# Performance work log

Hardware: AMD Instinct MI355X
Metric: run time of the kernel (lower is better)

Reference implementation:

```python
import jax, jax.numpy as jnp
import numpy as np

N = 50000      # nodes
E = 800000     # edges
IN = 128       # in_dim
EMB = 32       # emb_dim
ED = 8         # edge_dim
L = 4          # num_layers
B = 64         # num graphs in batch
OUT = 10       # out_dim
EPS = 1e-5


def setup_inputs() -> dict:
    key = jax.random.key(0)
    ks = jax.random.split(key, 16)
    f32 = jnp.float32
    def nrm(k, shape, scale):
        return jax.random.normal(k, shape, dtype=f32) * scale
    inp = {}
    inp['x'] = nrm(ks[0], (N, IN), 1.0)
    inp['edge_index'] = jax.random.randint(ks[1], (2, E), 0, N)
    inp['edge_attr'] = nrm(ks[2], (E, ED), 1.0)
    inp['batch'] = jnp.sort(jax.random.randint(ks[3], (N,), 0, B))
    # lin_in
    inp['lin_in_w'] = nrm(ks[4], (IN, EMB), 0.05)
    inp['lin_in_b'] = jnp.zeros((EMB,), f32)
    # per-layer message MLP: Linear(2e+ed->e), BN, ReLU, Linear(e->e), BN, ReLU
    inp['msg_w1'] = nrm(ks[5], (L, 2 * EMB + ED, EMB), 0.1)
    inp['msg_b1'] = jnp.zeros((L, EMB), f32)
    inp['msg_g1'] = jnp.ones((L, EMB), f32)
    inp['msg_be1'] = jnp.zeros((L, EMB), f32)
    inp['msg_w2'] = nrm(ks[6], (L, EMB, EMB), 0.1)
    inp['msg_b2'] = jnp.zeros((L, EMB), f32)
    inp['msg_g2'] = jnp.ones((L, EMB), f32)
    inp['msg_be2'] = jnp.zeros((L, EMB), f32)
    # per-layer update MLP: Linear(2e->e), BN, ReLU, Linear(e->e), BN, ReLU
    inp['upd_w1'] = nrm(ks[7], (L, 2 * EMB, EMB), 0.1)
    inp['upd_b1'] = jnp.zeros((L, EMB), f32)
    inp['upd_g1'] = jnp.ones((L, EMB), f32)
    inp['upd_be1'] = jnp.zeros((L, EMB), f32)
    inp['upd_w2'] = nrm(ks[8], (L, EMB, EMB), 0.1)
    inp['upd_b2'] = jnp.zeros((L, EMB), f32)
    inp['upd_g2'] = jnp.ones((L, EMB), f32)
    inp['upd_be2'] = jnp.zeros((L, EMB), f32)
    # lin_pred
    inp['pred_w'] = nrm(ks[9], (EMB, OUT), 0.1)
    inp['pred_b'] = jnp.zeros((OUT,), f32)
    return inp


def _bn(x, g, b):
    # BatchNorm1d in training mode: batch stats over dim 0 (biased variance)
    mu = jnp.mean(x, axis=0)
    var = jnp.mean(jnp.square(x - mu), axis=0)
    return (x - mu) * jax.lax.rsqrt(var + EPS) * g + b


def reference(x, edge_attr, lin_in_w, lin_in_b,
              msg_w1, msg_b1, msg_g1, msg_be1, msg_w2, msg_b2, msg_g2, msg_be2,
              upd_w1, upd_b1, upd_g1, upd_be1, upd_w2, upd_b2, upd_g2, upd_be2,
              pred_w, pred_b, edge_index, batch):
    src = edge_index[0]  # h_j source nodes
    dst = edge_index[1]  # h_i target nodes (aggregation index)
    h = x @ lin_in_w + lin_in_b  # [N, EMB]
    for i in range(L):
        # message: gather + concat + MLP(BN,ReLU)x2 over edges
        msg_in = jnp.concatenate([h[dst], h[src], edge_attr], axis=-1)  # [E, 2e+ed]
        m = jax.nn.relu(_bn(msg_in @ msg_w1[i] + msg_b1[i], msg_g1[i], msg_be1[i]))
        m = jax.nn.relu(_bn(m @ msg_w2[i] + msg_b2[i], msg_g2[i], msg_be2[i]))
        # aggregate: scatter-add by destination
        aggr = jax.ops.segment_sum(m, dst, num_segments=N)  # [N, EMB]
        # update: concat + MLP(BN,ReLU)x2
        u = jnp.concatenate([h, aggr], axis=-1)  # [N, 2e]
        u = jax.nn.relu(_bn(u @ upd_w1[i] + upd_b1[i], upd_g1[i], upd_be1[i]))
        u = jax.nn.relu(_bn(u @ upd_w2[i] + upd_b2[i], upd_g2[i], upd_be2[i]))
        h = u + h  # residual in MPNNModel.get_embeddings
    # global mean pool
    sums = jax.ops.segment_sum(h, batch, num_segments=B)
    counts = jax.ops.segment_sum(jnp.ones((N,), h.dtype), batch, num_segments=B)
    h_graph = sums / jnp.maximum(counts, 1.0)[:, None]
    return h_graph @ pred_w + pred_b  # [B, OUT]
```

## Files before the change

### kernel.cpp

```cpp
#include <hip/hip_runtime.h>
#include <cstddef>

#define N_NODES 50000
#define N_EDGES 800000
#define IN_DIM  128
#define EMB     32
#define ED      8
#define NLAYERS 4
#define NB      64
#define OUTD    10
#define EPS_BN  1e-5f

#define EDGE_GRID 3125
#define NODE_GRID 196
#define NODE4_GRID 782
#define AU_GRID   6250
#define NTILE_N   3125
#define LIN_GRID  782
#define ST_TPW    4
#define ST_GRID   3125
#define MSG2_TPW  4
#define MSG2_GRID 3125

#define SREP 4

typedef short bf16x8 __attribute__((ext_vector_type(8)));
typedef float f32x4  __attribute__((ext_vector_type(4)));


__device__ __forceinline__ unsigned short f2bf(float x) {
  union { float f; unsigned u; } v; v.f = x;
  unsigned b = v.u + 0x7FFFu + ((v.u >> 16) & 1u);
  return (unsigned short)(b >> 16);
}
__device__ __forceinline__ float bf2f(unsigned short s) {
  union { unsigned u; float f; } v; v.u = ((unsigned)s) << 16;
  return v.f;
}

__device__ __forceinline__ void coef_from_stats(const float* __restrict__ stats_stage,
                                                const float* __restrict__ g,
                                                const float* __restrict__ be,
                                                float inv_count, float* __restrict__ cf) {
  if (threadIdx.x < EMB) {
    const int c = threadIdx.x;
    float s = 0.f, ss = 0.f;
#pragma unroll
    for (int r = 0; r < SREP; ++r) {
      s  += stats_stage[r*64 + c];
      ss += stats_stage[r*64 + EMB + c];
    }
    const float mu  = s * inv_count;
    const float var = ss * inv_count - mu*mu;
    const float a = g[c] * rsqrtf(var + EPS_BN);
    cf[c] = a;
    cf[EMB + c] = fmaf(-mu, a, be[c]);
  }
  __syncthreads();
}

__device__ __forceinline__ void wave_stats_atomic(float ts[8], float tss[8],
                                                  float* __restrict__ lds_s,
                                                  float* __restrict__ lds_q,
                                                  float* __restrict__ stats_stage) {
  const int lane = threadIdx.x & 63;
  const int wv   = threadIdx.x >> 6;
#pragma unroll
  for (int j = 0; j < 8; ++j) {
    float a = ts[j], b = tss[j];
#pragma unroll
    for (int o = 32; o > 0; o >>= 1) {
      a += __shfl_down(a, o, 64);
      b += __shfl_down(b, o, 64);
    }
    ts[j] = a; tss[j] = b;
  }
  if (lane == 0) {
#pragma unroll
    for (int j = 0; j < 8; ++j) {
      lds_s[wv*8 + j] = ts[j];
      lds_q[wv*8 + j] = tss[j];
    }
  }
  __syncthreads();
  if (threadIdx.x < 64) {
    const float v = (threadIdx.x < 32) ? lds_s[threadIdx.x] : lds_q[threadIdx.x - 32];
    atomicAdd(stats_stage + ((blockIdx.x & (SREP-1)) << 6) + threadIdx.x, v);
  }
}

#define HSTRIDE 40

__global__ __launch_bounds__(256) void k_lin_in_pq(
    const float* __restrict__ x, const float* __restrict__ w, const float* __restrict__ b,
    const float* __restrict__ w1, const float* __restrict__ b1, const int* __restrict__ ei,
    float* __restrict__ h, unsigned short* __restrict__ p, unsigned short* __restrict__ q,
    int* __restrict__ cnt)
{
  __shared__ __align__(16) unsigned short lds_hb[4][16*HSTRIDE];
  __shared__ __align__(16) unsigned short lds_pq[4][16*HSTRIDE];
  const int lane = threadIdx.x & 63;
  const int wv   = threadIdx.x >> 6;
  const int n0i  = lane & 15;
  const int quad = lane >> 4;

  const int tile = blockIdx.x*4 + wv;
  if (tile < NTILE_N) {
    const int r0 = tile*16;
    bf16x8 BwL[4], BwH[4];
#pragma unroll
    for (int kb = 0; kb < 4; ++kb) {
#pragma unroll
      for (int j = 0; j < 8; ++j) {
        const int k = kb*32 + quad*8 + j;
        BwL[kb][j] = (short)f2bf(w[k*EMB + n0i]);
        BwH[kb][j] = (short)f2bf(w[k*EMB + 16 + n0i]);
      }
    }
    f32x4 accL = {0.f,0.f,0.f,0.f};
    f32x4 accH = {0.f,0.f,0.f,0.f};
#pragma unroll
    for (int kb = 0; kb < 4; ++kb) {
      const float4 xa = *(const float4*)(x + (size_t)(r0 + n0i)*IN_DIM + kb*32 + quad*8);
      const float4 xb = *(const float4*)(x + (size_t)(r0 + n0i)*IN_DIM + kb*32 + quad*8 + 4);
      bf16x8 A;
      A[0] = (short)f2bf(xa.x); A[1] = (short)f2bf(xa.y);
      A[2] = (short)f2bf(xa.z); A[3] = (short)f2bf(xa.w);
      A[4] = (short)f2bf(xb.x); A[5] = (short)f2bf(xb.y);
      A[6] = (short)f2bf(xb.z); A[7] = (short)f2bf(xb.w);
      accL = __builtin_amdgcn_mfma_f32_16x16x32_bf16(A, BwL[kb], accL, 0, 0, 0);
      accH = __builtin_amdgcn_mfma_f32_16x16x32_bf16(A, BwH[kb], accH, 0, 0, 0);
    }
    const float bL = b[n0i], bH = b[16 + n0i];
#pragma unroll
    for (int r = 0; r < 4; ++r) {
      const int row = quad*4 + r;
      const float vL = accL[r] + bL;
      const float vH = accH[r] + bH;
      h[(size_t)(r0 + row)*EMB + n0i]      = vL;
      h[(size_t)(r0 + row)*EMB + 16 + n0i] = vH;
      lds_hb[wv][row*HSTRIDE + n0i]      = f2bf(vL);
      lds_hb[wv][row*HSTRIDE + 16 + n0i] = f2bf(vH);
    }
    bf16x8 A2;
#pragma unroll
    for (int j = 0; j < 8; ++j)
      A2[j] = (short)lds_hb[wv][n0i*HSTRIDE + quad*8 + j];
    bf16x8 BpL, BpH, BqL, BqH;
#pragma unroll
    for (int j = 0; j < 8; ++j) {
      const int k = quad*8 + j;
      BpL[j] = (short)f2bf(w1[k*EMB + n0i]);
      BpH[j] = (short)f2bf(w1[k*EMB + 16 + n0i]);
      BqL[j] = (short)f2bf(w1[(EMB + k)*EMB + n0i]);
      BqH[j] = (short)f2bf(w1[(EMB + k)*EMB + 16 + n0i]);
    }
    const f32x4 z4 = {0.f,0.f,0.f,0.f};
    f32x4 pL = __builtin_amdgcn_mfma_f32_16x16x32_bf16(A2, BpL, z4, 0, 0, 0);
    f32x4 pH = __builtin_amdgcn_mfma_f32_16x16x32_bf16(A2, BpH, z4, 0, 0, 0);
    f32x4 qL = __builtin_amdgcn_mfma_f32_16x16x32_bf16(A2, BqL, z4, 0, 0, 0);
    f32x4 qH = __builtin_amdgcn_mfma_f32_16x16x32_bf16(A2, BqH, z4, 0, 0, 0);
    const float b1L = b1[n0i], b1H = b1[16 + n0i];
#pragma unroll
    for (int r = 0; r < 4; ++r) {
      const int row = quad*4 + r;
      lds_pq[wv][row*HSTRIDE + n0i]      = f2bf(pL[r] + b1L);
      lds_pq[wv][row*HSTRIDE + 16 + n0i] = f2bf(pH[r] + b1H);
    }
    {
      const int row2 = lane >> 2;
      const int c8   = (lane & 3)*8;
      const uint4 ov = *(const uint4*)&lds_pq[wv][row2*HSTRIDE + c8];
      *(uint4*)(p + (size_t)(r0 + row2)*EMB + c8) = ov;
    }
#pragma unroll
    for (int r = 0; r < 4; ++r) {
      const int row = quad*4 + r;
      lds_pq[wv][row*HSTRIDE + n0i]      = f2bf(qL[r]);
      lds_pq[wv][row*HSTRIDE + 16 + n0i] = f2bf(qH[r]);
    }
    {
      const int row2 = lane >> 2;
      const int c8   = (lane & 3)*8;
      const uint4 ov = *(const uint4*)&lds_pq[wv][row2*HSTRIDE + c8];
      *(uint4*)(q + (size_t)(r0 + row2)*EMB + c8) = ov;
    }
  }
  for (int e = blockIdx.x*256 + threadIdx.x; e < N_EDGES; e += gridDim.x*256)
    atomicAdd(&cnt[ei[N_EDGES + e]], 1);
}

__global__ __launch_bounds__(256) void k_scan_a(const int* __restrict__ cnt,
                                                int* __restrict__ row_ptr, int* __restrict__ bsum) {
  __shared__ int s[256];
  const int gid = blockIdx.x*256 + threadIdx.x;
  const int v = (gid < N_NODES) ? cnt[gid] : 0;
  s[threadIdx.x] = v;
  __syncthreads();
  for (int o = 1; o < 256; o <<= 1) {
    const int t = (threadIdx.x >= o) ? s[threadIdx.x - o] : 0;
    __syncthreads();
    s[threadIdx.x] += t;
    __syncthreads();
  }
  if (gid < N_NODES) row_ptr[gid] = s[threadIdx.x] - v;
  if (threadIdx.x == 255) bsum[blockIdx.x] = s[255];
}

__global__ __launch_bounds__(256) void k_scan_bc(int* __restrict__ row_ptr,
                                                 const int* __restrict__ bsum) {
  __shared__ int s[256];
  const int t = threadIdx.x;
  const int v = (t < NODE_GRID) ? bsum[t] : 0;
  s[t] = v;
  __syncthreads();
  for (int o = 1; o < 256; o <<= 1) {
    const int tt = (t >= o) ? s[t - o] : 0;
    __syncthreads();
    s[t] += tt;
    __syncthreads();
  }
  const int off = (blockIdx.x == 0) ? 0 : s[blockIdx.x - 1];
  const int gid = blockIdx.x*256 + t;
  if (gid < N_NODES) row_ptr[gid] += off;
  if (blockIdx.x == 0 && t == 0) row_ptr[N_NODES] = N_EDGES;
}

__global__ __launch_bounds__(256) void k_place_scatter(
    const int* __restrict__ ei, const float* __restrict__ ea,
    const int* __restrict__ row_ptr, int* __restrict__ cnt2,
    uint4* __restrict__ rec)
{
  const int e = blockIdx.x*256 + threadIdx.x;
  const int s = ei[e];
  const int d = ei[N_EDGES + e];
  const int pos = row_ptr[d] + atomicAdd(&cnt2[d], 1);
  const float4 v0 = ((const float4*)(ea + (size_t)e*ED))[0];
  const float4 v1 = ((const float4*)(ea + (size_t)e*ED))[1];
  const float ev[8] = {v0.x, v0.y, v0.z, v0.w, v1.x, v1.y, v1.z, v1.w};
  unsigned u[4];
#pragma unroll
  for (int j = 0; j < 4; ++j)
    u[j] = (unsigned)f2bf(ev[2*j]) | ((unsigned)f2bf(ev[2*j+1]) << 16);
  uint4* rp = rec + (size_t)pos*2;
  rp[0] = make_uint4((unsigned)s, (unsigned)d, u[0], u[1]);
  rp[1] = make_uint4(u[2], u[3], 0u, 0u);
}


__global__ __launch_bounds__(256) void k_stats1(
    const unsigned short* __restrict__ pb, const unsigned short* __restrict__ qb,
    const uint4* __restrict__ rec, const float* __restrict__ w1b,
    float* __restrict__ stats)
{
  __shared__ float lds_d[4][16*33];
  __shared__ float lds_s[4][32], lds_q[4][32];
  const int lane = threadIdx.x & 63;
  const int wv   = threadIdx.x >> 6;
  const int l15  = lane & 15;
  const int quad = lane >> 4;

  bf16x8 B1lo = {}, B1hi = {};
  if (quad == 0) {
#pragma unroll
    for (int j = 0; j < 8; ++j) {
      B1lo[j] = (short)f2bf(w1b[j*EMB + l15]);
      B1hi[j] = (short)f2bf(w1b[j*EMB + 16 + l15]);
    }
  }

  const int tile0 = blockIdx.x * (4*ST_TPW);
  uint4 RA[ST_TPW], RB[ST_TPW];
#pragma unroll
  for (int t = 0; t < ST_TPW; ++t) {
    const int tile = tile0 + t*4 + wv;
    const size_t e0 = (size_t)tile * 16;
    const uint4* r4 = rec + (e0 + l15)*2;
    RA[t] = r4[0];
    RB[t] = (quad == 0) ? r4[1] : make_uint4(0u,0u,0u,0u);
  }
  uint4 PG[ST_TPW], QG[ST_TPW];
#pragma unroll
  for (int t = 0; t < ST_TPW; ++t) {
    PG[t] = *(const uint4*)(pb + (size_t)RA[t].y*EMB + quad*8);
    QG[t] = *(const uint4*)(qb + (size_t)RA[t].x*EMB + quad*8);
  }

  float ts[8], tss[8];
#pragma unroll
  for (int j = 0; j < 8; ++j) { ts[j] = 0.f; tss[j] = 0.f; }

#pragma unroll
  for (int t = 0; t < ST_TPW; ++t) {
    bf16x8 A = {};
    if (quad == 0) {
      A[0] = (short)(RA[t].z & 0xFFFFu); A[1] = (short)(RA[t].z >> 16);
      A[2] = (short)(RA[t].w & 0xFFFFu); A[3] = (short)(RA[t].w >> 16);
      A[4] = (short)(RB[t].x & 0xFFFFu); A[5] = (short)(RB[t].x >> 16);
      A[6] = (short)(RB[t].y & 0xFFFFu); A[7] = (short)(RB[t].y >> 16);
    }
    const f32x4 z4 = {0.f,0.f,0.f,0.f};
    f32x4 D0 = __builtin_amdgcn_mfma_f32_16x16x32_bf16(A, B1lo, z4, 0, 0, 0);
    f32x4 D1 = __builtin_amdgcn_mfma_f32_16x16x32_bf16(A, B1hi, z4, 0, 0, 0);
#pragma unroll
    for (int r = 0; r < 4; ++r) {
      const int row = quad*4 + r;
      lds_d[wv][row*33 + l15]      = D0[r];
      lds_d[wv][row*33 + 16 + l15] = D1[r];
    }
    const unsigned pu[4] = {PG[t].x, PG[t].y, PG[t].z, PG[t].w};
    const unsigned qu[4] = {QG[t].x, QG[t].y, QG[t].z, QG[t].w};
#pragma unroll
    for (int jj = 0; jj < 4; ++jj) {
      const float d0 = lds_d[wv][l15*33 + quad*8 + 2*jj];
      const float d1 = lds_d[wv][l15*33 + quad*8 + 2*jj + 1];
      const float v0 = (d0 + bf2f((unsigned short)(pu[jj] & 0xFFFFu)))
                            + bf2f((unsigned short)(qu[jj] & 0xFFFFu));
      const float v1 = (d1 + bf2f((unsigned short)(pu[jj] >> 16)))
                            + bf2f((unsigned short)(qu[jj] >> 16));
      const float w0 = bf2f(f2bf(v0));
      const float w1v = bf2f(f2bf(v1));
      ts[2*jj]   += w0;  tss[2*jj]   = fmaf(w0, w0, tss[2*jj]);
      ts[2*jj+1] += w1v; tss[2*jj+1] = fmaf(w1v, w1v, tss[2*jj+1]);
    }
  }

#pragma unroll
  for (int j = 0; j < 8; ++j) {
    float a = ts[j], b = tss[j];
#pragma unroll
    for (int o = 1; o < 16; o <<= 1) {
      a += __shfl_xor(a, o, 64);
      b += __shfl_xor(b, o, 64);
    }
    ts[j] = a; tss[j] = b;
  }
  if (l15 == 0) {
#pragma unroll
    for (int j = 0; j < 8; ++j) {
      lds_s[wv][quad*8 + j] = ts[j];
      lds_q[wv][quad*8 + j] = tss[j];
    }
  }
  __syncthreads();
  if (threadIdx.x < 64) {
    const int c = threadIdx.x & 31;
    const int kind = threadIdx.x >> 5;
    float v = 0.f;
#pragma unroll
    for (int wq = 0; wq < 4; ++wq)
      v += kind ? lds_q[wq][c] : lds_s[wq][c];
    atomicAdd(stats + ((blockIdx.x & (SREP-1)) << 6) + kind*32 + c, v);
  }
}

__global__ __launch_bounds__(256) void k_msg2(
    const unsigned short* __restrict__ pb, const unsigned short* __restrict__ qb,
    const uint4* __restrict__ rec, const float* __restrict__ w1b,
    const float* __restrict__ stats1, const float* __restrict__ g1, const float* __restrict__ be1,
    const float* __restrict__ w2, const float* __restrict__ b2,
    unsigned short* __restrict__ y, float* __restrict__ stats2)
{
  __shared__ float lds_d[4][16*33];
  __shared__ __align__(16) unsigned short lds_t[4][16*32];
  __shared__ float lds_s[4][32], lds_q[4][32];
  __shared__ float cf[64];

  coef_from_stats(stats1, g1, be1, 1.0f/(float)N_EDGES, cf);

  const int lane = threadIdx.x & 63;
  const int wv   = threadIdx.x >> 6;
  const int l15  = lane & 15;
  const int quad = lane >> 4;

  bf16x8 B1lo = {}, B1hi = {};
  if (quad == 0) {
#pragma unroll
    for (int j = 0; j < 8; ++j) {
      B1lo[j] = (short)f2bf(w1b[j*EMB + l15]);
      B1hi[j] = (short)f2bf(w1b[j*EMB + 16 + l15]);
    }
  }
  bf16x8 Blo, Bhi;
#pragma unroll
  for (int j = 0; j < 8; ++j) {
    Blo[j] = (short)f2bf(w2[(quad*8 + j)*EMB + l15]);
    Bhi[j] = (short)f2bf(w2[(quad*8 + j)*EMB + 16 + l15]);
  }
  float a1[8], c1[8];
#pragma unroll
  for (int j = 0; j < 8; ++j) {
    a1[j] = cf[quad*8 + j];
    c1[j] = cf[EMB + quad*8 + j];
  }
  const float b2c0 = b2[l15], b2c1 = b2[16 + l15];

  float ts[8], tss[8];
#pragma unroll
  for (int j = 0; j < 8; ++j) { ts[j] = 0.f; tss[j] = 0.f; }

  const int tile0 = blockIdx.x * (4*MSG2_TPW);

  uint4 cRA, cRB, cPG, cQG;
  {
    const size_t e0 = (size_t)(tile0 + wv) * 16;
    const uint4* r4 = rec + (e0 + l15)*2;
    cRA = r4[0];
    cRB = (quad == 0) ? r4[1] : make_uint4(0u,0u,0u,0u);
    cPG = *(const uint4*)(pb + (size_t)cRA.y*EMB + quad*8);
    cQG = *(const uint4*)(qb + (size_t)cRA.x*EMB + quad*8);
  }

#pragma unroll
  for (int t = 0; t < MSG2_TPW; ++t) {
    const size_t e0 = (size_t)(tile0 + t*4 + wv) * 16;

    uint4 nRA = make_uint4(0u,0u,0u,0u), nRB = make_uint4(0u,0u,0u,0u);
    uint4 nPG = make_uint4(0u,0u,0u,0u), nQG = make_uint4(0u,0u,0u,0u);
    if (t + 1 < MSG2_TPW) {
      const size_t e1 = (size_t)(tile0 + (t+1)*4 + wv) * 16;
      const uint4* r4 = rec + (e1 + l15)*2;
      nRA = r4[0];
      nRB = (quad == 0) ? r4[1] : make_uint4(0u,0u,0u,0u);
    }

    bf16x8 A = {};
    if (quad == 0) {
      A[0] = (short)(cRA.z & 0xFFFFu); A[1] = (short)(cRA.z >> 16);
      A[2] = (short)(cRA.w & 0xFFFFu); A[3] = (short)(cRA.w >> 16);
      A[4] = (short)(cRB.x & 0xFFFFu); A[5] = (short)(cRB.x >> 16);
      A[6] = (short)(cRB.y & 0xFFFFu); A[7] = (short)(cRB.y >> 16);
    }
    const f32x4 z4 = {0.f,0.f,0.f,0.f};
    f32x4 D0 = __builtin_amdgcn_mfma_f32_16x16x32_bf16(A, B1lo, z4, 0, 0, 0);
    f32x4 D1 = __builtin_amdgcn_mfma_f32_16x16x32_bf16(A, B1hi, z4, 0, 0, 0);
#pragma unroll
    for (int r = 0; r < 4; ++r) {
      const int row = quad*4 + r;
      lds_d[wv][row*33 + l15]      = D0[r];
      lds_d[wv][row*33 + 16 + l15] = D1[r];
    }

    if (t + 1 < MSG2_TPW) {
      nPG = *(const uint4*)(pb + (size_t)nRA.y*EMB + quad*8);
      nQG = *(const uint4*)(qb + (size_t)nRA.x*EMB + quad*8);
    }

    const unsigned pu[4] = {cPG.x, cPG.y, cPG.z, cPG.w};
    const unsigned qu[4] = {cQG.x, cQG.y, cQG.z, cQG.w};
    bf16x8 A2;
#pragma unroll
    for (int jj = 0; jj < 4; ++jj) {
      const float d0 = lds_d[wv][l15*33 + quad*8 + 2*jj];
      const float d1 = lds_d[wv][l15*33 + quad*8 + 2*jj + 1];
      const float v0 = (d0 + bf2f((unsigned short)(pu[jj] & 0xFFFFu)))
                            + bf2f((unsigned short)(qu[jj] & 0xFFFFu));
      const float v1 = (d1 + bf2f((unsigned short)(pu[jj] >> 16)))
                            + bf2f((unsigned short)(qu[jj] >> 16));
      const float w0 = bf2f(f2bf(v0));
      const float w1v = bf2f(f2bf(v1));
      const float r0 = fmaxf(fmaf(a1[2*jj],   w0,  c1[2*jj]),   0.f);
      const float r1 = fmaxf(fmaf(a1[2*jj+1], w1v, c1[2*jj+1]), 0.f);
      A2[2*jj]   = (short)f2bf(r0);
      A2[2*jj+1] = (short)f2bf(r1);
    }

    f32x4 acc0 = {0.f, 0.f, 0.f, 0.f};
    f32x4 acc1 = {0.f, 0.f, 0.f, 0.f};
    acc0 = __builtin_amdgcn_mfma_f32_16x16x32_bf16(A2, Blo, acc0, 0, 0, 0);
    acc1 = __builtin_amdgcn_mfma_f32_16x16x32_bf16(A2, Bhi, acc1, 0, 0, 0);

#pragma unroll
    for (int r = 0; r < 4; ++r) {
      const int row = quad*4 + r;
      lds_t[wv][row*32 + l15]      = f2bf(acc0[r] + b2c0);
      lds_t[wv][row*32 + 16 + l15] = f2bf(acc1[r] + b2c1);
    }
    const uint4 orow = *(const uint4*)&lds_t[wv][(lane>>2)*32 + (lane&3)*8];
    *(uint4*)(y + (e0 + (lane>>2))*EMB + (lane&3)*8) = orow;

    const unsigned uo[4] = {orow.x, orow.y, orow.z, orow.w};
#pragma unroll
    for (int j = 0; j < 4; ++j) {
      const float v0 = bf2f((unsigned short)(uo[j] & 0xFFFFu));
      const float v1 = bf2f((unsigned short)(uo[j] >> 16));
      ts[2*j]   += v0;  tss[2*j]   = fmaf(v0, v0, tss[2*j]);
      ts[2*j+1] += v1;  tss[2*j+1] = fmaf(v1, v1, tss[2*j+1]);
    }

    cRA = nRA; cRB = nRB; cPG = nPG; cQG = nQG;
  }

#pragma unroll
  for (int j = 0; j < 8; ++j) {
    float s = ts[j], qq = tss[j];
#pragma unroll
    for (int o = 4; o < 64; o <<= 1) {
      s  += __shfl_xor(s, o, 64);
      qq += __shfl_xor(qq, o, 64);
    }
    ts[j] = s; tss[j] = qq;
  }
  if (lane < 4) {
#pragma unroll
    for (int j = 0; j < 8; ++j) {
      lds_s[wv][lane*8 + j] = ts[j];
      lds_q[wv][lane*8 + j] = tss[j];
    }
  }
  __syncthreads();
  if (threadIdx.x < 64) {
    const int c = threadIdx.x & 31;
    const int kind = threadIdx.x >> 5;
    float v = 0.f;
#pragma unroll
    for (int wq = 0; wq < 4; ++wq)
      v += kind ? lds_q[wq][c] : lds_s[wq][c];
    atomicAdd(stats2 + ((blockIdx.x & (SREP-1)) << 6) + kind*32 + c, v);
  }
}

__global__ __launch_bounds__(256) void k_aggr_upd1(
    const unsigned short* __restrict__ y, const int* __restrict__ row_ptr,
    const float* __restrict__ h,
    const float* __restrict__ stats1, const float* __restrict__ g2, const float* __restrict__ be2,
    const float* __restrict__ uw1, const float* __restrict__ ub1,
    float* __restrict__ z, float* __restrict__ stats2)
{
  __shared__ float cf[64];
  __shared__ float lh[8][32];
  __shared__ float la[8][32];
  __shared__ float rs[4][32], rq[4][32];
  coef_from_stats(stats1, g2, be2, 1.0f/(float)N_EDGES, cf);

  const int g = threadIdx.x >> 5;
  const int l = threadIdx.x & 31;
  const int n = blockIdx.x*8 + g;

  lh[g][l] = h[(size_t)n*EMB + l];

  const int rof = l >> 4;
  const int cp  = l & 15;
  const float a0 = cf[2*cp],     b0 = cf[EMB + 2*cp];
  const float a1 = cf[2*cp + 1], b1 = cf[EMB + 2*cp + 1];
  const int lo = row_ptr[n], hi = row_ptr[n+1];
  float s0 = 0.f, s1 = 0.f;
  for (int i = lo + rof; i < hi; i += 2) {
    const unsigned u = *(const unsigned*)(y + (size_t)i*EMB + 2*cp);
    const float v0 = bf2f((unsigned short)(u & 0xFFFFu));
    const float v1 = bf2f((unsigned short)(u >> 16));
    s0 += fmaxf(fmaf(a0, v0, b0), 0.f);
    s1 += fmaxf(fmaf(a1, v1, b1), 0.f);
  }
  s0 += __shfl_xor(s0, 16, 64);
  s1 += __shfl_xor(s1, 16, 64);
  if (rof == 0) { la[g][2*cp] = s0; la[g][2*cp + 1] = s1; }
  __syncthreads();

  float acc = ub1[l];
#pragma unroll
  for (int k = 0; k < EMB; ++k) acc = fmaf(lh[g][k], uw1[k*EMB + l], acc);
#pragma unroll
  for (int k = 0; k < EMB; ++k) acc = fmaf(la[g][k], uw1[(EMB + k)*EMB + l], acc);
  z[(size_t)n*EMB + l] = acc;

  const float sq = acc*acc;
  const float a2 = acc + __shfl_down(acc, 32, 64);
  const float q2 = sq  + __shfl_down(sq,  32, 64);
  const int wv = threadIdx.x >> 6;
  if ((threadIdx.x & 63) < 32) { rs[wv][l] = a2; rq[wv][l] = q2; }
  __syncthreads();
  if (threadIdx.x < 64) {
    const int c = threadIdx.x & 31;
    const int kind = threadIdx.x >> 5;
    float v = 0.f;
#pragma unroll
    for (int wq = 0; wq < 4; ++wq)
      v += kind ? rq[wq][c] : rs[wq][c];
    atomicAdd(stats2 + ((blockIdx.x & (SREP-1)) << 6) + kind*32 + c, v);
  }
}

__global__ __launch_bounds__(256) void k_upd2(
    float* __restrict__ z,
    const float* __restrict__ stats1, const float* __restrict__ g1, const float* __restrict__ be1,
    const float* __restrict__ w, const float* __restrict__ b,
    float* __restrict__ stats2)
{
  __shared__ float cf[64];
  __shared__ float lds_s[32], lds_q[32];
  coef_from_stats(stats1, g1, be1, 1.0f/(float)N_NODES, cf);

  const int lane = threadIdx.x & 63;
  const int wv   = threadIdx.x >> 6;
  const int n  = blockIdx.x*64 + lane;
  const int c0 = wv*8;
  float acc[8];
#pragma unroll
  for (int j = 0; j < 8; ++j) acc[j] = 0.f;
  if (n < N_NODES) {
#pragma unroll
    for (int j = 0; j < 8; ++j) acc[j] = b[c0 + j];
    const float4* zp = (const float4*)(z + (size_t)n*EMB);
#pragma unroll
    for (int k4 = 0; k4 < 8; ++k4) {
      const float4 v = zp[k4];
      const float mv[4] = {v.x, v.y, v.z, v.w};
#pragma unroll
      for (int t = 0; t < 4; ++t) {
        const int k = 4*k4 + t;
        const float m = fmaxf(fmaf(cf[k], mv[t], cf[EMB + k]), 0.f);
        const float* wk = w + k*EMB + c0;
#pragma unroll
        for (int j = 0; j < 8; ++j) acc[j] = fmaf(m, wk[j], acc[j]);
      }
    }
  }
  float ts[8], tss[8];
#pragma unroll
  for (int j = 0; j < 8; ++j) { ts[j] = acc[j]; tss[j] = acc[j]*acc[j]; }
  wave_stats_atomic(ts, tss, lds_s, lds_q, stats2);
  if (n < N_NODES) {
    float4 o0, o1;
    o0.x = acc[0]; o0.y = acc[1]; o0.z = acc[2]; o0.w = acc[3];
    o1.x = acc[4]; o1.y = acc[5]; o1.z = acc[6]; o1.w = acc[7];
    *(float4*)(z + (size_t)n*EMB + c0)     = o0;
    *(float4*)(z + (size_t)n*EMB + c0 + 4) = o1;
  }
}

__global__ __launch_bounds__(256) void k_resid_pq(
    float* __restrict__ h, const float* __restrict__ z,
    const float* __restrict__ stats, const float* __restrict__ g, const float* __restrict__ be,
    const float* __restrict__ w1_next, const float* __restrict__ b1_next,
    unsigned short* __restrict__ p, unsigned short* __restrict__ q)
{
  __shared__ float cf[64];
  __shared__ float lds_h[64][33];
  coef_from_stats(stats, g, be, 1.0f/(float)N_NODES, cf);

  const int lane = threadIdx.x & 63;
  const int wv   = threadIdx.x >> 6;
  const int n  = blockIdx.x*64 + lane;
  const int c0 = wv*8;
  if (n < N_NODES) {
    const float4* zp = (const float4*)(z + (size_t)n*EMB + c0);
    float4* hp = (float4*)(h + (size_t)n*EMB + c0);
    float hn[8];
    const float4 z0 = zp[0], z1 = zp[1];
    const float4 h0 = hp[0], h1 = hp[1];
    const float zv[8] = {z0.x, z0.y, z0.z, z0.w, z1.x, z1.y, z1.z, z1.w};
    const float hv[8] = {h0.x, h0.y, h0.z, h0.w, h1.x, h1.y, h1.z, h1.w};
#pragma unroll
    for (int j = 0; j < 8; ++j) {
      const int k = c0 + j;
      hn[j] = hv[j] + fmaxf(fmaf(cf[k], zv[j], cf[EMB + k]), 0.f);
      lds_h[lane][k] = hn[j];
    }
    float4 o0, o1;
    o0.x = hn[0]; o0.y = hn[1]; o0.z = hn[2]; o0.w = hn[3];
    o1.x = hn[4]; o1.y = hn[5]; o1.z = hn[6]; o1.w = hn[7];
    hp[0] = o0; hp[1] = o1;
  }
  __syncthreads();
  if (n < N_NODES && w1_next) {
    float ap[8], aq[8];
#pragma unroll
    for (int j = 0; j < 8; ++j) { ap[j] = b1_next[c0 + j]; aq[j] = 0.f; }
#pragma unroll
    for (int k = 0; k < EMB; ++k) {
      const float hvv = lds_h[lane][k];
      const float* wp = w1_next + k*EMB + c0;
      const float* wq = w1_next + (EMB + k)*EMB + c0;
#pragma unroll
      for (int j = 0; j < 8; ++j) ap[j] = fmaf(hvv, wp[j], ap[j]);
#pragma unroll
      for (int j = 0; j < 8; ++j) aq[j] = fmaf(hvv, wq[j], aq[j]);
    }
    unsigned up[4], uq[4];
#pragma unroll
    for (int j = 0; j < 4; ++j) {
      up[j] = (unsigned)f2bf(ap[2*j]) | ((unsigned)f2bf(ap[2*j+1]) << 16);
      uq[j] = (unsigned)f2bf(aq[2*j]) | ((unsigned)f2bf(aq[2*j+1]) << 16);
    }
    uint4 op; op.x = up[0]; op.y = up[1]; op.z = up[2]; op.w = up[3];
    uint4 oq; oq.x = uq[0]; oq.y = uq[1]; oq.z = uq[2]; oq.w = uq[3];
    *(uint4*)(p + (size_t)n*EMB + c0) = op;
    *(uint4*)(q + (size_t)n*EMB + c0) = oq;
  }
}

__global__ void k_pool(const float* __restrict__ h, const int* __restrict__ batch,
                       const float* __restrict__ pw, const float* __restrict__ pb,
                       float* __restrict__ out)
{
  __shared__ float sred[256];
  __shared__ float hg[EMB];
  const int b = blockIdx.x;
  int lo = 0, hi = N_NODES;
  while (lo < hi) { int m = (lo + hi) >> 1; if (batch[m] < b) lo = m + 1; else hi = m; }
  const int start = lo;
  hi = N_NODES;
  while (lo < hi) { int m = (lo + hi) >> 1; if (batch[m] < b + 1) lo = m + 1; else hi = m; }
  const int end = lo;

  const int c = threadIdx.x & (EMB-1);
  const int r = threadIdx.x >> 5;
  float s = 0.f;
  for (int n = start + r; n < end; n += 8) s += h[(size_t)n*EMB + c];
  sred[threadIdx.x] = s;
  __syncthreads();
  if (threadIdx.x < EMB) {
    float tot = 0.f;
#pragma unroll
    for (int r2 = 0; r2 < 8; ++r2) tot += sred[r2*EMB + threadIdx.x];
    const float cnt = (float)(end - start);
    hg[threadIdx.x] = tot / fmaxf(cnt, 1.f);
  }
  __syncthreads();
  if (threadIdx.x < OUTD) {
    float acc = pb[threadIdx.x];
#pragma unroll
    for (int cc = 0; cc < EMB; ++cc) acc = fmaf(hg[cc], pw[cc*OUTD + threadIdx.x], acc);
    out[b*OUTD + threadIdx.x] = acc;
  }
}


extern "C" void kernel_launch(void* const* d_in, const int* in_sizes, int n_in,
                              void* d_out, int out_size, void* d_ws, size_t ws_size,
                              hipStream_t stream) {
  const float* x        = (const float*)d_in[0];
  const int*   ei       = (const int*)  d_in[1];
  const float* ea       = (const float*)d_in[2];
  const int*   batch    = (const int*)  d_in[3];
  const float* lin_in_w = (const float*)d_in[4];
  const float* lin_in_b = (const float*)d_in[5];
  const float* msg_w1   = (const float*)d_in[6];
  const float* msg_b1   = (const float*)d_in[7];
  const float* msg_g1   = (const float*)d_in[8];
  const float* msg_be1  = (const float*)d_in[9];
  const float* msg_w2   = (const float*)d_in[10];
  const float* msg_b2   = (const float*)d_in[11];
  const float* msg_g2   = (const float*)d_in[12];
  const float* msg_be2  = (const float*)d_in[13];
  const float* upd_w1   = (const float*)d_in[14];
  const float* upd_b1   = (const float*)d_in[15];
  const float* upd_g1   = (const float*)d_in[16];
  const float* upd_be1  = (const float*)d_in[17];
  const float* upd_w2   = (const float*)d_in[18];
  const float* upd_b2   = (const float*)d_in[19];
  const float* upd_g2   = (const float*)d_in[20];
  const float* upd_be2  = (const float*)d_in[21];
  const float* pred_w   = (const float*)d_in[22];
  const float* pred_b   = (const float*)d_in[23];
  float* out = (float*)d_out;

  char* wsb = (char*)d_ws;
  unsigned short* y  = (unsigned short*)wsb;
  uint4* rec = (uint4*)(wsb + (size_t)N_EDGES*EMB*2);
  unsigned short* p  = (unsigned short*)(rec + (size_t)N_EDGES*2);
  unsigned short* q  = p + (size_t)N_NODES*EMB;
  float* h       = (float*)(q + (size_t)N_NODES*EMB);
  float* z       = h + (size_t)N_NODES*EMB;
  float* stats   = z + (size_t)N_NODES*EMB;
  int*   cnt     = (int*)(stats + 16*SREP*64);
  int*   cnt2    = cnt + N_NODES;
  int*   row_ptr = cnt2 + N_NODES;
  int*   bsum    = row_ptr + N_NODES + 1;
  const size_t need = ((size_t)((char*)(bsum + 256) - wsb));
  if (ws_size < need) return;

  hipMemsetAsync(stats, 0, (16*SREP*64 + 2*N_NODES)*sizeof(float), stream);

  k_lin_in_pq<<<LIN_GRID, 256, 0, stream>>>(x, lin_in_w, lin_in_b, msg_w1, msg_b1, ei,
                                            h, p, q, cnt);
  k_scan_a<<<NODE_GRID, 256, 0, stream>>>(cnt, row_ptr, bsum);
  k_scan_bc<<<NODE_GRID, 256, 0, stream>>>(row_ptr, bsum);
  k_place_scatter<<<EDGE_GRID, 256, 0, stream>>>(ei, ea, row_ptr, cnt2, rec);

  for (int l = 0; l < NLAYERS; ++l) {
    const int st = l*4;
    const float* w1  = msg_w1 + (size_t)l*(2*EMB+ED)*EMB;
    const float* w1b = w1 + (size_t)2*EMB*EMB;
    const float* w2  = msg_w2 + (size_t)l*EMB*EMB;
    const float* uw1 = upd_w1 + (size_t)l*(2*EMB)*EMB;
    const float* uw2 = upd_w2 + (size_t)l*EMB*EMB;
    const float* w1_next = (l+1 < NLAYERS) ? msg_w1 + (size_t)(l+1)*(2*EMB+ED)*EMB : nullptr;
    const float* b1_next = (l+1 < NLAYERS) ? msg_b1 + (size_t)(l+1)*EMB : nullptr;

    k_stats1<<<ST_GRID, 256, 0, stream>>>(p, q, rec, w1b, stats + (size_t)st*SREP*64);
    k_msg2<<<MSG2_GRID, 256, 0, stream>>>(p, q, rec, w1b,
                                          stats + (size_t)st*SREP*64,
                                          msg_g1 + l*EMB, msg_be1 + l*EMB,
                                          w2, msg_b2 + l*EMB,
                                          y, stats + (size_t)(st+1)*SREP*64);
    k_aggr_upd1<<<AU_GRID, 256, 0, stream>>>(y, row_ptr, h,
                                             stats + (size_t)(st+1)*SREP*64,
                                             msg_g2 + l*EMB, msg_be2 + l*EMB,
                                             uw1, upd_b1 + l*EMB,
                                             z, stats + (size_t)(st+2)*SREP*64);
    k_upd2<<<NODE4_GRID, 256, 0, stream>>>(z, stats + (size_t)(st+2)*SREP*64,
                                           upd_g1 + l*EMB, upd_be1 + l*EMB,
                                           uw2, upd_b2 + l*EMB, stats + (size_t)(st+3)*SREP*64);
    k_resid_pq<<<NODE4_GRID, 256, 0, stream>>>(h, z, stats + (size_t)(st+3)*SREP*64,
                                               upd_g2 + l*EMB, upd_be2 + l*EMB,
                                               w1_next, b1_next, p, q);
  }

  k_pool<<<NB, 256, 0, stream>>>(h, batch, pred_w, pred_b, out);
}
```

Measured before the change: 826.5 us.

## Split edge placement and fuse record permutation with layer-0 stats pass

The scatter-placement kernel now records only an inverse permutation (sorted slot to original edge index). A new kernel walks sorted slots, gathers the edge's src, dst and attributes, writes the packed record coalesced, and computes the layer-0 first-BN statistics in the same pass, so the separate layer-0 stats kernel is skipped. This replaces scattered 32-byte record writes with a 4-byte scattered write plus gathered reads, and saves one full edge sweep. It adds an inv buffer and a gathered read of ei and ea.

```diff
diff --git a/kernel.cpp b/kernel.cpp
--- a/kernel.cpp
+++ b/kernel.cpp
@@ -226,25 +226,138 @@
   if (blockIdx.x == 0 && t == 0) row_ptr[N_NODES] = N_EDGES;
 }
 
-__global__ __launch_bounds__(256) void k_place_scatter(
-    const int* __restrict__ ei, const float* __restrict__ ea,
-    const int* __restrict__ row_ptr, int* __restrict__ cnt2,
-    uint4* __restrict__ rec)
+__global__ __launch_bounds__(256) void k_place(
+    const int* __restrict__ ei, const int* __restrict__ row_ptr, int* __restrict__ cnt2,
+    int* __restrict__ inv)
 {
   const int e = blockIdx.x*256 + threadIdx.x;
-  const int s = ei[e];
   const int d = ei[N_EDGES + e];
   const int pos = row_ptr[d] + atomicAdd(&cnt2[d], 1);
-  const float4 v0 = ((const float4*)(ea + (size_t)e*ED))[0];
-  const float4 v1 = ((const float4*)(ea + (size_t)e*ED))[1];
-  const float ev[8] = {v0.x, v0.y, v0.z, v0.w, v1.x, v1.y, v1.z, v1.w};
-  unsigned u[4];
-#pragma unroll
-  for (int j = 0; j < 4; ++j)
-    u[j] = (unsigned)f2bf(ev[2*j]) | ((unsigned)f2bf(ev[2*j+1]) << 16);
-  uint4* rp = rec + (size_t)pos*2;
-  rp[0] = make_uint4((unsigned)s, (unsigned)d, u[0], u[1]);
-  rp[1] = make_uint4(u[2], u[3], 0u, 0u);
+  inv[pos] = e;
+}
+
+__global__ __launch_bounds__(256) void k_permute_stats(
+    const int* __restrict__ inv, const int* __restrict__ ei, const float* __restrict__ ea,
+    const unsigned short* __restrict__ pb, const unsigned short* __restrict__ qb,
+    const float* __restrict__ w1b,
+    uint4* __restrict__ rec, float* __restrict__ stats)
+{
+  __shared__ float lds_d[4][16*33];
+  __shared__ unsigned lds_r[4][16*6];
+  __shared__ float lds_s[4][32], lds_q[4][32];
+  const int lane = threadIdx.x & 63;
+  const int wv   = threadIdx.x >> 6;
+  const int l15  = lane & 15;
+  const int quad = lane >> 4;
+
+  bf16x8 B1lo = {}, B1hi = {};
+  if (quad == 0) {
+#pragma unroll
+    for (int j = 0; j < 8; ++j) {
+      B1lo[j] = (short)f2bf(w1b[j*EMB + l15]);
+      B1hi[j] = (short)f2bf(w1b[j*EMB + 16 + l15]);
+    }
+  }
+
+  float ts[8], tss[8];
+#pragma unroll
+  for (int j = 0; j < 8; ++j) { ts[j] = 0.f; tss[j] = 0.f; }
+
+  const int tile0 = blockIdx.x * (4*ST_TPW);
+#pragma unroll
+  for (int t = 0; t < ST_TPW; ++t) {
+    const int tile = tile0 + t*4 + wv;
+    const int r0 = tile*16;
+
+    const int e   = inv[r0 + l15];
+    const int src = ei[e];
+    const int dst = ei[N_EDGES + e];
+
+    unsigned u0 = 0, u1 = 0, u2 = 0, u3 = 0;
+    if (quad == 0) {
+      const float4 v0 = ((const float4*)(ea + (size_t)e*ED))[0];
+      const float4 v1 = ((const float4*)(ea + (size_t)e*ED))[1];
+      u0 = (unsigned)f2bf(v0.x) | ((unsigned)f2bf(v0.y) << 16);
+      u1 = (unsigned)f2bf(v0.z) | ((unsigned)f2bf(v0.w) << 16);
+      u2 = (unsigned)f2bf(v1.x) | ((unsigned)f2bf(v1.y) << 16);
+      u3 = (unsigned)f2bf(v1.z) | ((unsigned)f2bf(v1.w) << 16);
+      unsigned* rr = &lds_r[wv][l15*6];
+      rr[0] = (unsigned)src; rr[1] = (unsigned)dst;
+      rr[2] = u0; rr[3] = u1; rr[4] = u2; rr[5] = u3;
+    }
+
+    bf16x8 A = {};
+    if (quad == 0) {
+      A[0] = (short)(u0 & 0xFFFFu); A[1] = (short)(u0 >> 16);
+      A[2] = (short)(u1 & 0xFFFFu); A[3] = (short)(u1 >> 16);
+      A[4] = (short)(u2 & 0xFFFFu); A[5] = (short)(u2 >> 16);
+      A[6] = (short)(u3 & 0xFFFFu); A[7] = (short)(u3 >> 16);
+    }
+    const f32x4 z4 = {0.f,0.f,0.f,0.f};
+    f32x4 D0 = __builtin_amdgcn_mfma_f32_16x16x32_bf16(A, B1lo, z4, 0, 0, 0);
+    f32x4 D1 = __builtin_amdgcn_mfma_f32_16x16x32_bf16(A, B1hi, z4, 0, 0, 0);
+#pragma unroll
+    for (int r = 0; r < 4; ++r) {
+      const int row = quad*4 + r;
+      lds_d[wv][row*33 + l15]      = D0[r];
+      lds_d[wv][row*33 + 16 + l15] = D1[r];
+    }
+
+    if (lane < 32) {
+      const int w = lane >> 1;
+      const unsigned* rr = &lds_r[wv][w*6];
+      if ((lane & 1) == 0)
+        rec[(size_t)(r0 + w)*2]     = make_uint4(rr[0], rr[1], rr[2], rr[3]);
+      else
+        rec[(size_t)(r0 + w)*2 + 1] = make_uint4(rr[4], rr[5], 0u, 0u);
+    }
+
+    const uint4 pg = *(const uint4*)(pb + (size_t)dst*EMB + quad*8);
+    const uint4 qg = *(const uint4*)(qb + (size_t)src*EMB + quad*8);
+    const unsigned pu[4] = {pg.x, pg.y, pg.z, pg.w};
+    const unsigned qu[4] = {qg.x, qg.y, qg.z, qg.w};
+#pragma unroll
+    for (int jj = 0; jj < 4; ++jj) {
+      const float d0 = lds_d[wv][l15*33 + quad*8 + 2*jj];
+      const float d1 = lds_d[wv][l15*33 + quad*8 + 2*jj + 1];
+      const float v0 = (d0 + bf2f((unsigned short)(pu[jj] & 0xFFFFu)))
+                            + bf2f((unsigned short)(qu[jj] & 0xFFFFu));
+      const float v1 = (d1 + bf2f((unsigned short)(pu[jj] >> 16)))
+                            + bf2f((unsigned short)(qu[jj] >> 16));
+      const float w0 = bf2f(f2bf(v0));
+      const float w1v = bf2f(f2bf(v1));
+      ts[2*jj]   += w0;  tss[2*jj]   = fmaf(w0, w0, tss[2*jj]);
+      ts[2*jj+1] += w1v; tss[2*jj+1] = fmaf(w1v, w1v, tss[2*jj+1]);
+    }
+  }
+
+#pragma unroll
+  for (int j = 0; j < 8; ++j) {
+    float a = ts[j], b = tss[j];
+#pragma unroll
+    for (int o = 1; o < 16; o <<= 1) {
+      a += __shfl_xor(a, o, 64);
+      b += __shfl_xor(b, o, 64);
+    }
+    ts[j] = a; tss[j] = b;
+  }
+  if (l15 == 0) {
+#pragma unroll
+    for (int j = 0; j < 8; ++j) {
+      lds_s[wv][quad*8 + j] = ts[j];
+      lds_q[wv][quad*8 + j] = tss[j];
+    }
+  }
+  __syncthreads();
+  if (threadIdx.x < 64) {
+    const int c = threadIdx.x & 31;
+    const int kind = threadIdx.x >> 5;
+    float v = 0.f;
+#pragma unroll
+    for (int wq = 0; wq < 4; ++wq)
+      v += kind ? lds_q[wq][c] : lds_s[wq][c];
+    atomicAdd(stats + ((blockIdx.x & (SREP-1)) << 6) + kind*32 + c, v);
+  }
 }
 
 
@@ -768,7 +881,8 @@
   int*   cnt2    = cnt + N_NODES;
   int*   row_ptr = cnt2 + N_NODES;
   int*   bsum    = row_ptr + N_NODES + 1;
-  const size_t need = ((size_t)((char*)(bsum + 256) - wsb));
+  int*   inv     = bsum + 256;
+  const size_t need = ((size_t)((char*)(inv + N_EDGES) - wsb));
   if (ws_size < need) return;
 
   hipMemsetAsync(stats, 0, (16*SREP*64 + 2*N_NODES)*sizeof(float), stream);
@@ -777,7 +891,10 @@
                                             h, p, q, cnt);
   k_scan_a<<<NODE_GRID, 256, 0, stream>>>(cnt, row_ptr, bsum);
   k_scan_bc<<<NODE_GRID, 256, 0, stream>>>(row_ptr, bsum);
-  k_place_scatter<<<EDGE_GRID, 256, 0, stream>>>(ei, ea, row_ptr, cnt2, rec);
+  k_place<<<EDGE_GRID, 256, 0, stream>>>(ei, row_ptr, cnt2, inv);
+  k_permute_stats<<<ST_GRID, 256, 0, stream>>>(inv, ei, ea, p, q,
+                                               msg_w1 + (size_t)2*EMB*EMB,
+                                               rec, stats);
 
   for (int l = 0; l < NLAYERS; ++l) {
     const int st = l*4;
@@ -789,7 +906,8 @@
     const float* w1_next = (l+1 < NLAYERS) ? msg_w1 + (size_t)(l+1)*(2*EMB+ED)*EMB : nullptr;
     const float* b1_next = (l+1 < NLAYERS) ? msg_b1 + (size_t)(l+1)*EMB : nullptr;
 
-    k_stats1<<<ST_GRID, 256, 0, stream>>>(p, q, rec, w1b, stats + (size_t)st*SREP*64);
+    if (l > 0)
+      k_stats1<<<ST_GRID, 256, 0, stream>>>(p, q, rec, w1b, stats + (size_t)st*SREP*64);
     k_msg2<<<MSG2_GRID, 256, 0, stream>>>(p, q, rec, w1b,
                                           stats + (size_t)st*SREP*64,
                                           msg_g1 + l*EMB, msg_be1 + l*EMB,
```

Measured after the change: 853.3 us. +3.2%, slower.
